# Kernel tuning notes

Measured on AMD Instinct MI355X. Metric: run time of the kernel, lower is better.

Reference implementation:

```python
import jax, jax.numpy as jnp
import numpy as np

EMBED = 4096
HEADS = 16
HEAD_DIM = EMBED // HEADS  # 256
ROT = 64                   # rotary_dim
B, S = 1, 2048
MASK_VAL = -1.0e9          # masked_bias


def setup_inputs() -> dict:
    key = jax.random.key(0)
    ks = jax.random.split(key, 5)
    sc = 0.02
    return {
        "hidden_states": jax.random.normal(ks[0], (B, S, EMBED), jnp.float32),
        "Wq": jax.random.normal(ks[1], (EMBED, EMBED), jnp.float32) * sc,
        "Wk": jax.random.normal(ks[2], (EMBED, EMBED), jnp.float32) * sc,
        "Wv": jax.random.normal(ks[3], (EMBED, EMBED), jnp.float32) * sc,
        "Wo": jax.random.normal(ks[4], (EMBED, EMBED), jnp.float32) * sc,
    }


def _rotate_every_two(x):
    # interleave: (x0,x1,x2,x3,...) -> (x1,x0,x3,x2,...)  [as written in source]
    r = jnp.stack((x[..., 1::2], x[..., ::2]), axis=-1)
    return r.reshape(x.shape)


def _fixed_pos_embedding(seq_len, rot_dim):
    inv_freq = 1.0 / (10000.0 ** (jnp.arange(0, rot_dim, 2, dtype=jnp.float32) / rot_dim))
    t = jnp.arange(seq_len, dtype=jnp.float32)
    sinusoid = jnp.einsum('i,j->ij', t, inv_freq)  # [S, rot_dim/2]
    return jnp.sin(sinusoid), jnp.cos(sinusoid)


def _apply_rotary(x, sin, cos):
    # x: [B, S, H, ROT]; sin/cos: [S, ROT/2] -> repeat each freq twice along last dim
    sin = jnp.repeat(sin[None, :, None, :], 2, axis=3)
    cos = jnp.repeat(cos[None, :, None, :], 2, axis=3)
    return x * cos + _rotate_every_two(x) * sin


def reference(hidden_states, Wq, Wk, Wv, Wo):
    b, s, e = hidden_states.shape
    q = (hidden_states @ Wq).reshape(b, s, HEADS, HEAD_DIM)
    k = (hidden_states @ Wk).reshape(b, s, HEADS, HEAD_DIM)
    v = (hidden_states @ Wv).reshape(b, s, HEADS, HEAD_DIM)

    sin, cos = _fixed_pos_embedding(s, ROT)
    q = jnp.concatenate([_apply_rotary(q[..., :ROT], sin, cos), q[..., ROT:]], axis=-1)
    k = jnp.concatenate([_apply_rotary(k[..., :ROT], sin, cos), k[..., ROT:]], axis=-1)

    q = q.transpose(0, 2, 1, 3)  # [B,H,S,D]
    k = k.transpose(0, 2, 1, 3)
    v = v.transpose(0, 2, 1, 3)

    logits = jnp.einsum('bhqd,bhkd->bhqk', q, k)  # [B,H,S,S]
    causal = jnp.tril(jnp.ones((s, s), dtype=bool))[None, None]
    # GPT-J quirk: mask applied BEFORE scaling
    logits = jnp.where(causal, logits, MASK_VAL)
    logits = logits / jnp.sqrt(jnp.float32(HEAD_DIM))
    attn = jax.nn.softmax(logits, axis=-1)

    out = jnp.einsum('bhqk,bhkd->bhqd', attn, v)
    out = out.transpose(0, 2, 1, 3).reshape(b, s, e)
    return out @ Wo
```

## Files before the change

### kernel.cpp

```cpp
#include <hip/hip_runtime.h>
#include <hip/hip_bf16.h>
#include <math.h>

#define EMBED 4096
#define SLEN 2048
#define HEADS 16
#define HDIM 256
#define ROT 64

typedef __bf16 bf16;
typedef __attribute__((ext_vector_type(8))) __bf16 bf16x8;
typedef __attribute__((ext_vector_type(4))) float f32x4;

__device__ __forceinline__ void async_copy16(const void* g, void* l) {
  __builtin_amdgcn_global_load_lds((const __attribute__((address_space(1))) void*)g,
                                   (__attribute__((address_space(3))) void*)l,
                                   16, 0, 0);
}

__global__ __launch_bounds__(256) void cast_kernel(const float* __restrict__ in,
                                                   bf16* __restrict__ out, int n4) {
  int i = blockIdx.x * 256 + threadIdx.x;
  if (i >= n4) return;
  float4 v = ((const float4*)in)[i];
  bf16 o[4] __attribute__((aligned(8)));
  o[0] = (bf16)v.x; o[1] = (bf16)v.y; o[2] = (bf16)v.z; o[3] = (bf16)v.w;
  ((ushort4*)out)[i] = *(const ushort4*)o;
}

__device__ __forceinline__ void transpose_body(const float* __restrict__ W,
                                               bf16* __restrict__ Wt) {
  __shared__ bf16 tile[64][65];
  int k0 = blockIdx.y * 64, n0 = blockIdx.x * 64;
  int tr = threadIdx.x >> 4, tc = threadIdx.x & 15;
#pragma unroll
  for (int i = 0; i < 4; i++) {
    int row = tr + i * 16;
    float4 v = *(const float4*)(W + (size_t)(k0 + row) * EMBED + n0 + tc * 4);
    tile[row][tc * 4 + 0] = (bf16)v.x;
    tile[row][tc * 4 + 1] = (bf16)v.y;
    tile[row][tc * 4 + 2] = (bf16)v.z;
    tile[row][tc * 4 + 3] = (bf16)v.w;
  }
  __syncthreads();
#pragma unroll
  for (int i = 0; i < 4; i++) {
    int nl = tr + i * 16;
    bf16 o[4] __attribute__((aligned(8)));
#pragma unroll
    for (int j = 0; j < 4; j++) o[j] = tile[tc * 4 + j][nl];
    *(ushort4*)(Wt + (size_t)(n0 + nl) * EMBED + k0 + tc * 4) = *(const ushort4*)o;
  }
}

__global__ __launch_bounds__(256) void transpose_cast(const float* __restrict__ W,
                                                      bf16* __restrict__ Wt) {
  transpose_body(W, Wt);
}

__global__ __launch_bounds__(256) void transpose_cast3(const float* __restrict__ Wq,
                                                       const float* __restrict__ Wk,
                                                       const float* __restrict__ Wv,
                                                       bf16* __restrict__ Wt3) {
  int z = blockIdx.z;
  const float* W = (z == 0) ? Wq : (z == 1) ? Wk : Wv;
  transpose_body(W, Wt3 + (size_t)z * EMBED * EMBED);
}

__global__ __launch_bounds__(256) void transpose_cast4(const float* __restrict__ Wq,
                                                       const float* __restrict__ Wk,
                                                       const float* __restrict__ Wv,
                                                       const float* __restrict__ Wo,
                                                       bf16* __restrict__ Wt4) {
  int z = blockIdx.z;
  const float* W = (z == 0) ? Wq : (z == 1) ? Wk : (z == 2) ? Wv : Wo;
  transpose_body(W, Wt4 + (size_t)z * EMBED * EMBED);
}

__device__ __forceinline__ void gemm_body(const bf16* __restrict__ A,
                                          const bf16* __restrict__ Bt,
                                          void* __restrict__ Cout,
                                          int M, int N, int K, int mode,
                                          int bx, int by) {
  constexpr int BM = 128, BN = 256, BK = 64;
  __shared__ __align__(16) bf16 As[3][BM * BK];
  __shared__ __align__(16) bf16 Bs[3][BN * BK];
  int t = threadIdx.x;
  int lane = t & 63, w = t >> 6;
  int c16 = lane & 15, g4 = lane >> 4;
  int wm = w >> 2, wn = w & 3;
  int m0 = by * BM, n0 = bx * BN;
  int nt = K / BK;

  f32x4 acc[4][4] = {};

  auto stage = [&](int kt, int slot) {
    const bf16* Asrc = A + (size_t)m0 * K + kt * BK;
    const bf16* Bsrc = Bt + (size_t)n0 * K + kt * BK;
    bf16* Ad = As[slot];
    bf16* Bd = Bs[slot];
#pragma unroll
    for (int i = 0; i < 2; i++) {
      int c = i * 512 + t;
      int row = c >> 3, col8 = c & 7;
      async_copy16(Asrc + (size_t)row * K + ((col8 ^ (row & 7)) * 8), Ad + c * 8);
    }
#pragma unroll
    for (int i = 0; i < 4; i++) {
      int c = i * 512 + t;
      int row = c >> 3, col8 = c & 7;
      async_copy16(Bsrc + (size_t)row * K + ((col8 ^ (row & 7)) * 8), Bd + c * 8);
    }
  };

  stage(0, 0);
  stage(1, 1);
  asm volatile("s_waitcnt vmcnt(6)" ::: "memory");
  __builtin_amdgcn_s_barrier();

  for (int kt = 0; kt < nt; kt++) {
    int slot = kt - (kt / 3) * 3;
    const bf16* Ab = As[slot];
    const bf16* Bb = Bs[slot];

    bf16x8 af[2][4], bfr[2][4];
#pragma unroll
    for (int kk = 0; kk < 2; kk++) {
#pragma unroll
      for (int fm = 0; fm < 4; fm++) {
        int row = wm * 64 + fm * 16 + c16;
        af[kk][fm] = *(const bf16x8*)(Ab + row * BK + (((kk * 4 + g4) ^ (row & 7)) * 8));
      }
#pragma unroll
      for (int fn = 0; fn < 4; fn++) {
        int row = wn * 64 + fn * 16 + c16;
        bfr[kk][fn] = *(const bf16x8*)(Bb + row * BK + (((kk * 4 + g4) ^ (row & 7)) * 8));
      }
    }
    if (kt + 2 < nt) {
      int s2 = (kt + 2) - ((kt + 2) / 3) * 3;
      stage(kt + 2, s2);
    }
    __builtin_amdgcn_s_setprio(1);
#pragma unroll
    for (int kk = 0; kk < 2; kk++)
#pragma unroll
      for (int fm = 0; fm < 4; fm++)
#pragma unroll
        for (int fn = 0; fn < 4; fn++)
          acc[fm][fn] = __builtin_amdgcn_mfma_f32_16x16x32_bf16(af[kk][fm], bfr[kk][fn],
                                                                acc[fm][fn], 0, 0, 0);
    __builtin_amdgcn_s_setprio(0);
    if (kt < nt - 2) {
      asm volatile("s_waitcnt vmcnt(6)" ::: "memory");
      __builtin_amdgcn_s_barrier();
    } else if (kt == nt - 2) {
      asm volatile("s_waitcnt vmcnt(0)" ::: "memory");
      __builtin_amdgcn_s_barrier();
    }
  }

#pragma unroll
  for (int fm = 0; fm < 4; fm++) {
#pragma unroll
    for (int fn = 0; fn < 4; fn++) {
      int col = n0 + wn * 64 + fn * 16 + c16;
#pragma unroll
      for (int r = 0; r < 4; r++) {
        int row = m0 + wm * 64 + fm * 16 + g4 * 4 + r;
        float v = acc[fm][fn][r];
        if (mode == 1) {
          int d = col & (HDIM - 1);
          if (d < ROT) {
            float pv = __shfl_xor(v, 1);
            int jj = d >> 1;
            float invf = __expf(-0.28782313662425575f * (float)jj);
            float ang = (float)row * invf;
            float sa, ca;
            sincosf(ang, &sa, &ca);
            v = v * ca + pv * sa;
          }
        }
        if (mode == 3) {
          ((float*)Cout)[(size_t)row * N + col] = v;
        } else if (mode == 2) {
          ((bf16*)Cout)[(size_t)col * M + row] = (bf16)v;
        } else {
          ((bf16*)Cout)[(size_t)row * N + col] = (bf16)v;
        }
      }
    }
  }
}

template <int MODE>
__global__ __launch_bounds__(512, 1) void gemm_pipe(const bf16* __restrict__ A,
                                                    const bf16* __restrict__ Bt,
                                                    void* __restrict__ Cout,
                                                    int M, int N, int K) {
  int l = blockIdx.x + 16 * blockIdx.y;
  int xcd = l & 7, i = l >> 3;
  int p = i >> 4, by = i & 15;
  int bx = xcd * 2 + p;
  gemm_body(A, Bt, Cout, M, N, K, MODE, bx, by);
}

__global__ __launch_bounds__(512, 1) void gemm_qkv(const bf16* __restrict__ A,
                                                   const bf16* __restrict__ Wt3,
                                                   bf16* __restrict__ Qb,
                                                   bf16* __restrict__ Kb,
                                                   bf16* __restrict__ Vtb) {
  int l = blockIdx.x + 16 * blockIdx.y + 256 * blockIdx.z;
  int xcd = l & 7, i = l >> 3;
  int p = i >> 4, by = i & 15;
  int pid = xcd * 6 + p;
  int z = pid >> 4;
  int bx = pid & 15;
  const bf16* Bt = Wt3 + (size_t)z * EMBED * EMBED;
  void* out = (z == 0) ? (void*)Qb : (z == 1) ? (void*)Kb : (void*)Vtb;
  int mode = (z == 2) ? 2 : 1;
  gemm_body(A, Bt, out, SLEN, EMBED, EMBED, mode, bx, by);
}

__global__ __launch_bounds__(256, 2) void attn_kernel(const bf16* __restrict__ Q,
                                                      const bf16* __restrict__ Kmat,
                                                      const bf16* __restrict__ Vt,
                                                      bf16* __restrict__ O) {
  __shared__ __align__(16) bf16 Ks[64 * 256];
  __shared__ __align__(16) bf16 Vs[64 * 256];
  __shared__ __align__(16) bf16 Pl[4][16 * 64];
  int t = threadIdx.x, lane = t & 63, w = t >> 6;
  int c16 = lane & 15, g4 = lane >> 4;
  int b = blockIdx.x;
  int bb = b & 255;
  int h = bb & 15;
  int k = bb >> 4;
  int qt = (b >> 8) ? k : (31 - k);
  int q0w = qt * 64 + w * 16;

  auto stageK = [&](int kt) {
#pragma unroll
    for (int j = 0; j < 8; j++) {
      int c = j * 256 + t;
      int row = c >> 5, col8 = c & 31;
      async_copy16(Kmat + (size_t)(kt * 64 + row) * EMBED + h * HDIM +
                       ((col8 ^ (row & 7)) * 8),
                   Ks + (size_t)c * 8);
    }
  };
  auto stageV = [&](int kt) {
#pragma unroll
    for (int j = 0; j < 8; j++) {
      int c = j * 256 + t;
      int row = c >> 3, col8 = c & 7;
      async_copy16(Vt + (size_t)(h * HDIM + row) * SLEN + kt * 64 +
                       ((col8 ^ (row & 7)) * 8),
                   Vs + (size_t)c * 8);
    }
  };

  bf16x8 qf[8];
  {
    const bf16* qp = Q + (size_t)(q0w + c16) * EMBED + h * HDIM + g4 * 8;
#pragma unroll
    for (int kk = 0; kk < 8; kk++) qf[kk] = *(const bf16x8*)(qp + kk * 32);
  }
  f32x4 acco[16] = {};
  float mrow[4], lrow[4];
#pragma unroll
  for (int r = 0; r < 4; r++) { mrow[r] = -1e30f; lrow[r] = 0.f; }

  stageK(0);
  stageV(0);
  __syncthreads();

  for (int kt = 0; kt <= qt; kt++) {
    f32x4 accs[4] = {};
    __builtin_amdgcn_s_setprio(1);
#pragma unroll
    for (int kk = 0; kk < 8; kk++) {
#pragma unroll
      for (int fn = 0; fn < 4; fn++) {
        int r = fn * 16 + c16;
        bf16x8 kf = *(const bf16x8*)(Ks + r * 256 + ((kk * 4 + g4) ^ (c16 & 7)) * 8);
        accs[fn] = __builtin_amdgcn_mfma_f32_16x16x32_bf16(qf[kk], kf, accs[fn], 0, 0, 0);
      }
    }
    __builtin_amdgcn_s_setprio(0);
    __syncthreads();
    if (kt < qt) stageK(kt + 1);

    float pm[4][4];
    bool diag = (kt == qt);
#pragma unroll
    for (int fn = 0; fn < 4; fn++)
#pragma unroll
      for (int r = 0; r < 4; r++) {
        float s = accs[fn][r] * 0.0625f;
        if (diag) {
          int kg = fn * 16 + c16;
          int qg = w * 16 + g4 * 4 + r;
          if (kg > qg) s = -1e30f;
        }
        pm[fn][r] = s;
      }
    float lmax[4];
#pragma unroll
    for (int r = 0; r < 4; r++)
      lmax[r] = fmaxf(fmaxf(pm[0][r], pm[1][r]), fmaxf(pm[2][r], pm[3][r]));
    bool need = false;
#pragma unroll
    for (int r = 0; r < 4; r++) need = need || (lmax[r] > mrow[r] + 8.0f);
    if (__any(need)) {
#pragma unroll
      for (int r = 0; r < 4; r++) {
        float mx = lmax[r];
#pragma unroll
        for (int off = 1; off < 16; off <<= 1) mx = fmaxf(mx, __shfl_xor(mx, off));
        float mn = fmaxf(mrow[r], mx);
        float sc = __expf(mrow[r] - mn);
        mrow[r] = mn;
        lrow[r] *= sc;
#pragma unroll
        for (int fd = 0; fd < 16; fd++) acco[fd][r] *= sc;
      }
    }
#pragma unroll
    for (int fn = 0; fn < 4; fn++)
#pragma unroll
      for (int r = 0; r < 4; r++) {
        float p = __expf(pm[fn][r] - mrow[r]);
        pm[fn][r] = p;
        lrow[r] += p;
      }
#pragma unroll
    for (int fn = 0; fn < 4; fn++)
#pragma unroll
      for (int r = 0; r < 4; r++) {
        int q = g4 * 4 + r;
        int chunk = (fn * 2 + (c16 >> 3)) ^ (q & 7);
        Pl[w][q * 64 + chunk * 8 + (c16 & 7)] = (bf16)pm[fn][r];
      }
    __builtin_amdgcn_s_setprio(1);
#pragma unroll
    for (int kk2 = 0; kk2 < 2; kk2++) {
      bf16x8 pf = *(const bf16x8*)(&Pl[w][c16 * 64 + ((kk2 * 4 + g4) ^ (c16 & 7)) * 8]);
#pragma unroll
      for (int fd = 0; fd < 16; fd++) {
        int rv = fd * 16 + c16;
        bf16x8 vf = *(const bf16x8*)(Vs + rv * 64 + ((kk2 * 4 + g4) ^ (c16 & 7)) * 8);
        acco[fd] = __builtin_amdgcn_mfma_f32_16x16x32_bf16(pf, vf, acco[fd], 0, 0, 0);
      }
    }
    __builtin_amdgcn_s_setprio(0);
    __syncthreads();
    if (kt < qt) stageV(kt + 1);
  }
  float inv[4];
#pragma unroll
  for (int r = 0; r < 4; r++) {
    float s = lrow[r];
#pragma unroll
    for (int off = 1; off < 16; off <<= 1) s += __shfl_xor(s, off);
    inv[r] = 1.0f / s;
  }
#pragma unroll
  for (int fd = 0; fd < 16; fd++)
#pragma unroll
    for (int r = 0; r < 4; r++) {
      int qg = q0w + g4 * 4 + r;
      int col = h * HDIM + fd * 16 + c16;
      O[(size_t)qg * EMBED + col] = (bf16)(acco[fd][r] * inv[r]);
    }
}

extern "C" void kernel_launch(void* const* d_in, const int* in_sizes, int n_in,
                              void* d_out, int out_size, void* d_ws, size_t ws_size,
                              hipStream_t stream) {
  const float* hidden = (const float*)d_in[0];
  const float* Wq = (const float*)d_in[1];
  const float* Wk = (const float*)d_in[2];
  const float* Wv = (const float*)d_in[3];
  const float* Wo = (const float*)d_in[4];
  float* out = (float*)d_out;

  char* ws = (char*)d_ws;
  const size_t SZ_H = (size_t)SLEN * EMBED * 2;
  const size_t SZ_W = (size_t)EMBED * EMBED * 2;

  dim3 tgrid(EMBED / 64, EMBED / 64);
  dim3 ggrid(EMBED / 256, SLEN / 128);

  if (ws_size >= 5 * SZ_H + 4 * SZ_W) {
    bf16* h_bf = (bf16*)ws;
    bf16* Wt4  = (bf16*)(ws + SZ_H);
    bf16* Qb   = (bf16*)(ws + SZ_H + 4 * SZ_W);
    bf16* Kb   = (bf16*)(ws + 2 * SZ_H + 4 * SZ_W);
    bf16* Vtb  = (bf16*)(ws + 3 * SZ_H + 4 * SZ_W);
    bf16* Ob   = (bf16*)(ws + 4 * SZ_H + 4 * SZ_W);

    cast_kernel<<<(SLEN * EMBED / 4 + 255) / 256, 256, 0, stream>>>(
        hidden, h_bf, SLEN * EMBED / 4);
    transpose_cast4<<<dim3(EMBED / 64, EMBED / 64, 4), 256, 0, stream>>>(
        Wq, Wk, Wv, Wo, Wt4);
    gemm_qkv<<<dim3(EMBED / 256, SLEN / 128, 3), 512, 0, stream>>>(h_bf, Wt4, Qb,
                                                                   Kb, Vtb);
    attn_kernel<<<dim3(512), 256, 0, stream>>>(Qb, Kb, Vtb, Ob);
    gemm_pipe<3><<<ggrid, 512, 0, stream>>>(Ob, Wt4 + (size_t)3 * EMBED * EMBED,
                                            out, SLEN, EMBED, EMBED);
    return;
  }

  if (ws_size >= 5 * SZ_H + 3 * SZ_W) {
    bf16* h_bf = (bf16*)ws;
    bf16* Wt3  = (bf16*)(ws + SZ_H);
    bf16* Qb   = (bf16*)(ws + SZ_H + 3 * SZ_W);
    bf16* Kb   = (bf16*)(ws + 2 * SZ_H + 3 * SZ_W);
    bf16* Vtb  = (bf16*)(ws + 3 * SZ_H + 3 * SZ_W);
    bf16* Ob   = (bf16*)(ws + 4 * SZ_H + 3 * SZ_W);

    cast_kernel<<<(SLEN * EMBED / 4 + 255) / 256, 256, 0, stream>>>(
        hidden, h_bf, SLEN * EMBED / 4);
    transpose_cast3<<<dim3(EMBED / 64, EMBED / 64, 3), 256, 0, stream>>>(Wq, Wk,
                                                                         Wv, Wt3);
    gemm_qkv<<<dim3(EMBED / 256, SLEN / 128, 3), 512, 0, stream>>>(h_bf, Wt3, Qb,
                                                                   Kb, Vtb);
    attn_kernel<<<dim3(512), 256, 0, stream>>>(Qb, Kb, Vtb, Ob);
    transpose_cast<<<tgrid, 256, 0, stream>>>(Wo, Wt3);
    gemm_pipe<3><<<ggrid, 512, 0, stream>>>(Ob, Wt3, out, SLEN, EMBED, EMBED);
    return;
  }

  if (ws_size < 5 * SZ_H + SZ_W) return;
  bf16* h_bf = (bf16*)ws;
  bf16* Wt   = (bf16*)(ws + SZ_H);
  bf16* Qb   = (bf16*)(ws + SZ_H + SZ_W);
  bf16* Kb   = (bf16*)(ws + 2 * SZ_H + SZ_W);
  bf16* Vtb  = (bf16*)(ws + 3 * SZ_H + SZ_W);
  bf16* Ob   = (bf16*)(ws + 4 * SZ_H + SZ_W);

  cast_kernel<<<(SLEN * EMBED / 4 + 255) / 256, 256, 0, stream>>>(hidden, h_bf,
                                                                  SLEN * EMBED / 4);
  transpose_cast<<<tgrid, 256, 0, stream>>>(Wq, Wt);
  gemm_pipe<1><<<ggrid, 512, 0, stream>>>(h_bf, Wt, Qb, SLEN, EMBED, EMBED);
  transpose_cast<<<tgrid, 256, 0, stream>>>(Wk, Wt);
  gemm_pipe<1><<<ggrid, 512, 0, stream>>>(h_bf, Wt, Kb, SLEN, EMBED, EMBED);
  transpose_cast<<<tgrid, 256, 0, stream>>>(Wv, Wt);
  gemm_pipe<2><<<ggrid, 512, 0, stream>>>(h_bf, Wt, Vtb, SLEN, EMBED, EMBED);
  attn_kernel<<<dim3(512), 256, 0, stream>>>(Qb, Kb, Vtb, Ob);
  transpose_cast<<<tgrid, 256, 0, stream>>>(Wo, Wt);
  gemm_pipe<3><<<ggrid, 512, 0, stream>>>(Ob, Wt, out, SLEN, EMBED, EMBED);
}
```

Before: 451.5 us.

## Use dedicated 256x256-tile double-buffered GEMM for fused QKV projection

```diff
diff --git a/kernel.cpp b/kernel.cpp
--- a/kernel.cpp
+++ b/kernel.cpp
@@ -210,16 +210,106 @@
                                                    bf16* __restrict__ Qb,
                                                    bf16* __restrict__ Kb,
                                                    bf16* __restrict__ Vtb) {
-  int l = blockIdx.x + 16 * blockIdx.y + 256 * blockIdx.z;
-  int xcd = l & 7, i = l >> 3;
-  int p = i >> 4, by = i & 15;
-  int pid = xcd * 6 + p;
-  int z = pid >> 4;
-  int bx = pid & 15;
+  constexpr int BM = 256, BN = 256, BK = 64;
+  constexpr int M = SLEN, N = EMBED, K = EMBED;
+  __shared__ __align__(16) bf16 As[2][BM * BK];
+  __shared__ __align__(16) bf16 Bs[2][BN * BK];
+  int z = blockIdx.z;
   const bf16* Bt = Wt3 + (size_t)z * EMBED * EMBED;
-  void* out = (z == 0) ? (void*)Qb : (z == 1) ? (void*)Kb : (void*)Vtb;
+  void* Cout = (z == 0) ? (void*)Qb : (z == 1) ? (void*)Kb : (void*)Vtb;
   int mode = (z == 2) ? 2 : 1;
-  gemm_body(A, Bt, out, SLEN, EMBED, EMBED, mode, bx, by);
+
+  int t = threadIdx.x;
+  int lane = t & 63, w = t >> 6;
+  int c16 = lane & 15, g4 = lane >> 4;
+  int wm = w >> 2, wn = w & 3;
+  int m0 = blockIdx.y * BM, n0 = blockIdx.x * BN;
+  int nt = K / BK;
+
+  f32x4 acc[8][4] = {};
+
+  auto stage = [&](int kt, int slot) {
+    const bf16* Asrc = A + (size_t)m0 * K + kt * BK;
+    const bf16* Bsrc = Bt + (size_t)n0 * K + kt * BK;
+    bf16* Ad = As[slot];
+    bf16* Bd = Bs[slot];
+#pragma unroll
+    for (int i = 0; i < 4; i++) {
+      int c = i * 512 + t;
+      int row = c >> 3, col8 = c & 7;
+      async_copy16(Asrc + (size_t)row * K + ((col8 ^ (row & 7)) * 8), Ad + c * 8);
+    }
+#pragma unroll
+    for (int i = 0; i < 4; i++) {
+      int c = i * 512 + t;
+      int row = c >> 3, col8 = c & 7;
+      async_copy16(Bsrc + (size_t)row * K + ((col8 ^ (row & 7)) * 8), Bd + c * 8);
+    }
+  };
+
+  stage(0, 0);
+  asm volatile("s_waitcnt vmcnt(0)" ::: "memory");
+  __builtin_amdgcn_s_barrier();
+
+  for (int kt = 0; kt < nt; kt++) {
+    int slot = kt & 1;
+    if (kt + 1 < nt) stage(kt + 1, slot ^ 1);
+    const bf16* Ab = As[slot];
+    const bf16* Bb = Bs[slot];
+
+#pragma unroll
+    for (int kk = 0; kk < 2; kk++) {
+      bf16x8 bfr[4];
+#pragma unroll
+      for (int fn = 0; fn < 4; fn++) {
+        int row = wn * 64 + fn * 16 + c16;
+        bfr[fn] = *(const bf16x8*)(Bb + row * BK + (((kk * 4 + g4) ^ (row & 7)) * 8));
+      }
+      __builtin_amdgcn_s_setprio(1);
+#pragma unroll
+      for (int fm = 0; fm < 8; fm++) {
+        int row = wm * 128 + fm * 16 + c16;
+        bf16x8 afm = *(const bf16x8*)(Ab + row * BK + (((kk * 4 + g4) ^ (row & 7)) * 8));
+#pragma unroll
+        for (int fn = 0; fn < 4; fn++)
+          acc[fm][fn] = __builtin_amdgcn_mfma_f32_16x16x32_bf16(afm, bfr[fn],
+                                                                acc[fm][fn], 0, 0, 0);
+      }
+      __builtin_amdgcn_s_setprio(0);
+    }
+    asm volatile("s_waitcnt vmcnt(0)" ::: "memory");
+    __builtin_amdgcn_s_barrier();
+  }
+
+#pragma unroll
+  for (int fm = 0; fm < 8; fm++) {
+#pragma unroll
+    for (int fn = 0; fn < 4; fn++) {
+      int col = n0 + wn * 64 + fn * 16 + c16;
+#pragma unroll
+      for (int r = 0; r < 4; r++) {
+        int row = m0 + wm * 128 + fm * 16 + g4 * 4 + r;
+        float v = acc[fm][fn][r];
+        if (mode == 1) {
+          int d = col & (HDIM - 1);
+          if (d < ROT) {
+            float pv = __shfl_xor(v, 1);
+            int jj = d >> 1;
+            float invf = __expf(-0.28782313662425575f * (float)jj);
+            float ang = (float)row * invf;
+            float sa, ca;
+            sincosf(ang, &sa, &ca);
+            v = v * ca + pv * sa;
+          }
+        }
+        if (mode == 2) {
+          ((bf16*)Cout)[(size_t)col * M + row] = (bf16)v;
+        } else {
+          ((bf16*)Cout)[(size_t)row * N + col] = (bf16)v;
+        }
+      }
+    }
+  }
 }
 
 __global__ __launch_bounds__(256, 2) void attn_kernel(const bf16* __restrict__ Q,
@@ -390,6 +480,7 @@
 
   dim3 tgrid(EMBED / 64, EMBED / 64);
   dim3 ggrid(EMBED / 256, SLEN / 128);
+  dim3 qgrid(EMBED / 256, SLEN / 256, 3);
 
   if (ws_size >= 5 * SZ_H + 4 * SZ_W) {
     bf16* h_bf = (bf16*)ws;
@@ -403,8 +494,7 @@
         hidden, h_bf, SLEN * EMBED / 4);
     transpose_cast4<<<dim3(EMBED / 64, EMBED / 64, 4), 256, 0, stream>>>(
         Wq, Wk, Wv, Wo, Wt4);
-    gemm_qkv<<<dim3(EMBED / 256, SLEN / 128, 3), 512, 0, stream>>>(h_bf, Wt4, Qb,
-                                                                   Kb, Vtb);
+    gemm_qkv<<<qgrid, 512, 0, stream>>>(h_bf, Wt4, Qb, Kb, Vtb);
     attn_kernel<<<dim3(512), 256, 0, stream>>>(Qb, Kb, Vtb, Ob);
     gemm_pipe<3><<<ggrid, 512, 0, stream>>>(Ob, Wt4 + (size_t)3 * EMBED * EMBED,
                                             out, SLEN, EMBED, EMBED);
@@ -423,8 +513,7 @@
         hidden, h_bf, SLEN * EMBED / 4);
     transpose_cast3<<<dim3(EMBED / 64, EMBED / 64, 3), 256, 0, stream>>>(Wq, Wk,
                                                                          Wv, Wt3);
-    gemm_qkv<<<dim3(EMBED / 256, SLEN / 128, 3), 512, 0, stream>>>(h_bf, Wt3, Qb,
-                                                                   Kb, Vtb);
+    gemm_qkv<<<qgrid, 512, 0, stream>>>(h_bf, Wt3, Qb, Kb, Vtb);
     attn_kernel<<<dim3(512), 256, 0, stream>>>(Qb, Kb, Vtb, Ob);
     transpose_cast<<<tgrid, 256, 0, stream>>>(Wo, Wt3);
     gemm_pipe<3><<<ggrid, 512, 0, stream>>>(Ob, Wt3, out, SLEN, EMBED, EMBED);
```

New measurement: 563.2 us. 1.25x slower.
